# Kernel optimization log

Measured on AMD Instinct MI355X. Metric: run time of the kernel, lower is better.

## Reference

```python
import jax, jax.numpy as jnp
import numpy as np

B, S, E = 4, 4096, 1024
H, D, L = 16, 64, 64   # heads, head_dim, landmarks
KS = 33                # depthwise conv kernel size (seq dim)
N_ITER = 6


def setup_inputs() -> dict:
    key = jax.random.key(0)
    ks = jax.random.split(key, 8)
    s = 0.02
    return {
        "hidden_states": jax.random.normal(ks[0], (B, S, E), dtype=jnp.float32),
        "Wq": jax.random.normal(ks[1], (E, E), dtype=jnp.float32) * s,
        "bq": jnp.zeros((E,), dtype=jnp.float32),
        "Wk": jax.random.normal(ks[2], (E, E), dtype=jnp.float32) * s,
        "bk": jnp.zeros((E,), dtype=jnp.float32),
        "Wv": jax.random.normal(ks[3], (E, E), dtype=jnp.float32) * s,
        "bv": jnp.zeros((E,), dtype=jnp.float32),
        "conv_w": jax.random.normal(ks[4], (H, 1, KS, 1), dtype=jnp.float32) * 0.1,
    }


def _iterative_pinv_original(a, n_iter=N_ITER):
    # a: [B,H,L,L]. Faithful to _pinv_original_nystrom: GLOBAL max over all batches/heads.
    eye = jnp.eye(a.shape[-1], dtype=a.dtype)
    val = a.swapaxes(-1, -2) / jnp.max(jnp.sum(a, axis=-2))
    for _ in range(n_iter):
        kv = a @ val
        val = 0.25 * val @ (13.0 * eye - kv @ (15.0 * eye - kv @ (7.0 * eye - kv)))
    return val


def reference(hidden_states, Wq, bq, Wk, bk, Wv, bv, conv_w):
    scale = D ** -0.25  # divide q and k each by head_dim**0.25

    def heads(x):  # [B,S,E] -> [B,H,S,D]
        return x.reshape(B, S, H, D).transpose(0, 2, 1, 3)

    q = heads(hidden_states @ Wq + bq) * scale
    k = heads(hidden_states @ Wk + bk) * scale
    v = heads(hidden_states @ Wv + bv)

    # landmark means over segments of length S//L
    ql = q.reshape(B, H, L, S // L, D).mean(axis=-2)  # [B,H,L,D]
    kl = k.reshape(B, H, L, S // L, D).mean(axis=-2)  # [B,H,L,D]

    kernel_1 = jax.nn.softmax(jnp.einsum('bhsd,bhld->bhsl', q, kl), axis=-1)   # [B,H,S,L]
    kernel_2 = jax.nn.softmax(jnp.einsum('bhmd,bhld->bhml', ql, kl), axis=-1)  # [B,H,L,L]
    kernel_3 = jax.nn.softmax(jnp.einsum('bhld,bhsd->bhls', ql, k), axis=-1)   # [B,H,L,S]

    pinv = _iterative_pinv_original(kernel_2)
    attention_probs = kernel_1 @ pinv            # [B,H,S,L]
    new_value = kernel_3 @ v                     # [B,H,L,D]
    ctx = attention_probs @ new_value            # [B,H,S,D]

    # depthwise conv skip on value_layer: Conv2d(H,H,(KS,1),groups=H,bias=False)
    pad = KS // 2
    conv_out = jax.lax.conv_general_dilated(
        v, conv_w, window_strides=(1, 1), padding=((pad, pad), (0, 0)),
        dimension_numbers=('NCHW', 'OIHW', 'NCHW'), feature_group_count=H)
    ctx = ctx + conv_out

    return ctx.transpose(0, 2, 1, 3).reshape(B, S, H * D)
```

## Files before the change

kernel.cpp:

```cpp
#include <hip/hip_runtime.h>
#include <stdint.h>

typedef unsigned short u16;
typedef float f32x4 __attribute__((ext_vector_type(4)));
typedef __bf16 bf16x8 __attribute__((ext_vector_type(8)));
typedef u16 u16x8 __attribute__((ext_vector_type(8)));
typedef u16 u16x4 __attribute__((ext_vector_type(4)));

#define SCALE_QK 0.35355339059327373f

#define BAR() asm volatile("s_barrier" ::: "memory")
#define WAIT_LGKM0() do { asm volatile("s_waitcnt lgkmcnt(0)" ::: "memory"); __builtin_amdgcn_sched_barrier(0); } while (0)
#define WAIT_VM(n) do { asm volatile("s_waitcnt vmcnt(" #n ")" ::: "memory"); __builtin_amdgcn_sched_barrier(0); } while (0)

__device__ __forceinline__ u16 f2bf(float f) {
  union { float f; uint32_t u; } x; x.f = f;
  uint32_t r = x.u + 0x7fffu + ((x.u >> 16) & 1u);
  return (u16)(r >> 16);
}
__device__ __forceinline__ float bf2f(u16 h) {
  union { uint32_t u; float f; } x; x.u = ((uint32_t)h) << 16;
  return x.f;
}
__device__ __forceinline__ void gload16(const void* g, void* l) {
  __builtin_amdgcn_global_load_lds((const __attribute__((address_space(1))) void*)g,
                                   (__attribute__((address_space(3))) void*)l, 16, 0, 0);
}
__device__ __forceinline__ bf16x8 ld_f32_to_bf8(const float* p) {
  f32x4 a = *(const f32x4*)p, b = *(const f32x4*)(p + 4);
  union { u16x8 u; bf16x8 h; } c;
  c.u[0] = f2bf(a[0]); c.u[1] = f2bf(a[1]); c.u[2] = f2bf(a[2]); c.u[3] = f2bf(a[3]);
  c.u[4] = f2bf(b[0]); c.u[5] = f2bf(b[1]); c.u[6] = f2bf(b[2]); c.u[7] = f2bf(b[3]);
  return c.h;
}

__global__ __launch_bounds__(256) void k_prep(const float* __restrict__ hidden,
                                              const float* __restrict__ Wq, const float* __restrict__ Wk,
                                              const float* __restrict__ Wv,
                                              u16* __restrict__ hb, u16* __restrict__ Wt) {
  __shared__ float tile[64][65];
  const int bx = blockIdx.x;
  const int t = threadIdx.x;
  if (bx < 8192) {
    const size_t i = ((size_t)bx * 256 + t) * 8;
    f32x4 v0 = *(const f32x4*)(hidden + i);
    f32x4 v1 = *(const f32x4*)(hidden + i + 4);
    u16x8 o;
    o[0] = f2bf(v0[0]); o[1] = f2bf(v0[1]); o[2] = f2bf(v0[2]); o[3] = f2bf(v0[3]);
    o[4] = f2bf(v1[0]); o[5] = f2bf(v1[1]); o[6] = f2bf(v1[2]); o[7] = f2bf(v1[3]);
    *(u16x8*)(hb + i) = o;
    return;
  }
  const int bxx = bx - 8192;
  const int w = bxx >> 8, tn = (bxx >> 4) & 15, tk = bxx & 15;
  const float* W = (w == 0) ? Wq : ((w == 1) ? Wk : Wv);
  const int r = t >> 2, c0 = (t & 3) * 16;
  const float* src = W + (size_t)(tk * 64 + r) * 1024 + tn * 64 + c0;
#pragma unroll
  for (int j = 0; j < 16; j += 4) {
    f32x4 x = *(const f32x4*)(src + j);
    tile[r][c0 + j + 0] = x[0]; tile[r][c0 + j + 1] = x[1];
    tile[r][c0 + j + 2] = x[2]; tile[r][c0 + j + 3] = x[3];
  }
  __syncthreads();
  u16* dst = Wt + (size_t)(w * 1024 + tn * 64 + r) * 1024 + tk * 64 + c0;
#pragma unroll
  for (int j = 0; j < 16; ++j) dst[j] = f2bf(tile[c0 + j][r]);
}

__device__ __forceinline__ bf16x8 frg(const u16* buf, int row, int ks, int lhi) {
  const int ck = (ks << 2) + lhi;
  return *reinterpret_cast<const bf16x8*>(buf + (row << 6) + ((ck ^ (row & 7)) << 3));
}
__device__ __forceinline__ void issue(const u16* g, int rowbase, int tc, u16* ldsbase, int wid) {
  gload16(g + (((size_t)rowbase) << 10) + tc, ldsbase + ((rowbase + (wid << 3)) << 6));
}
template <int Q>
__device__ __forceinline__ void quad_mfma(const bf16x8 (&af)[2][2], const bf16x8 (&bf)[4][2],
                                          f32x4 (&acc)[8][4]) {
#pragma unroll
  for (int mm = 0; mm < 2; ++mm)
#pragma unroll
    for (int n = 0; n < 4; ++n) {
      acc[Q * 2 + mm][n] = __builtin_amdgcn_mfma_f32_16x16x32_bf16(af[mm][0], bf[n][0], acc[Q * 2 + mm][n], 0, 0, 0);
      acc[Q * 2 + mm][n] = __builtin_amdgcn_mfma_f32_16x16x32_bf16(af[mm][1], bf[n][1], acc[Q * 2 + mm][n], 0, 0, 0);
    }
}
#define LOADA_TO(dst, Q)                                     \
  dst[0][0] = frg(ASr, rA0 + (Q)*32, 0, lhi);                \
  dst[0][1] = frg(ASr, rA0 + (Q)*32, 1, lhi);                \
  dst[1][0] = frg(ASr, rA0 + (Q)*32 + 16, 0, lhi);           \
  dst[1][1] = frg(ASr, rA0 + (Q)*32 + 16, 1, lhi);

__global__ __launch_bounds__(512) void k_gemm2(const u16* __restrict__ A, const u16* __restrict__ Bt,
                                               const float* __restrict__ bq, const float* __restrict__ bk,
                                               const float* __restrict__ bv,
                                               u16* __restrict__ oq, u16* __restrict__ ok, u16* __restrict__ ov,
                                               float* __restrict__ ql, float* __restrict__ kl) {
  __shared__ __align__(16) u16 AS[2][256 * 64];
  __shared__ __align__(16) u16 BS[2][256 * 64];
  __shared__ __align__(16) u16 obuf[8][16][70];
  const int t = threadIdx.x, lane = t & 63, wid = t >> 6;
  const int wm = wid >> 2, wn = wid & 3;
  const int bm = blockIdx.x, bn = blockIdx.y;
  const int l15 = lane & 15, lhi = lane >> 4;

  const int rowoff = t >> 3;
  const int cswz = (t & 7) ^ (rowoff & 7);
  const u16* aG = A + (((size_t)(bm * 256 + rowoff)) << 10) + (cswz << 3);
  const u16* bG = Bt + (((size_t)(bn * 256 + rowoff)) << 10) + (cswz << 3);

  const int rA0 = wm * 128 + l15;
  const int rB0 = wn * 64 + l15;

  f32x4 acc[8][4];
#pragma unroll
  for (int m = 0; m < 8; ++m)
#pragma unroll
    for (int n = 0; n < 4; ++n) acc[m][n] = (f32x4){0.f, 0.f, 0.f, 0.f};

  issue(bG, 0, 0, BS[0], wid);
  issue(bG, 64, 0, BS[0], wid);
  issue(bG, 128, 0, BS[0], wid);
  issue(bG, 192, 0, BS[0], wid);
  issue(aG, 0, 0, AS[0], wid);
  issue(aG, 128, 0, AS[0], wid);
  issue(aG, 64, 0, AS[0], wid);
  issue(aG, 192, 0, AS[0], wid);
  WAIT_VM(2);
  BAR();

  for (int u = 0; u < 15; ++u) {
    const int pu = u & 1;
    const u16* ASr = AS[pu];
    const u16* BSr = BS[pu];
    u16* ASw = AS[pu ^ 1];
    u16* BSw = BS[pu ^ 1];
    const int tc = (u + 1) << 6;
    bf16x8 bfr[4][2];
    bf16x8 afA[2][2], afB[2][2];
#pragma unroll
    for (int n = 0; n < 4; ++n) {
      bfr[n][0] = frg(BSr, rB0 + n * 16, 0, lhi);
      bfr[n][1] = frg(BSr, rB0 + n * 16, 1, lhi);
    }
    LOADA_TO(afA, 0)
    LOADA_TO(afB, 1)
    issue(bG, 0, tc, BSw, wid);
    issue(bG, 64, tc, BSw, wid);
    issue(bG, 128, tc, BSw, wid);
    issue(bG, 192, tc, BSw, wid);
    issue(aG, 0, tc, ASw, wid);
    issue(aG, 128, tc, ASw, wid);
    issue(aG, 64, tc, ASw, wid);
    issue(aG, 192, tc, ASw, wid);
    __builtin_amdgcn_s_setprio(1);
    quad_mfma<0>(afA, bfr, acc);
    __builtin_amdgcn_s_setprio(0);
    WAIT_VM(8);
    BAR();
    LOADA_TO(afA, 2)
    __builtin_amdgcn_s_setprio(1);
    quad_mfma<1>(afB, bfr, acc);
    __builtin_amdgcn_s_setprio(0);
    LOADA_TO(afB, 3)
    __builtin_amdgcn_s_setprio(1);
    quad_mfma<2>(afA, bfr, acc);
    __builtin_amdgcn_s_setprio(0);
    __builtin_amdgcn_s_setprio(1);
    quad_mfma<3>(afB, bfr, acc);
    __builtin_amdgcn_s_setprio(0);
    WAIT_VM(2);
    BAR();
  }
  {
    const u16* ASr = AS[1];
    const u16* BSr = BS[1];
    bf16x8 bfr[4][2];
    bf16x8 afA[2][2], afB[2][2];
#pragma unroll
    for (int n = 0; n < 4; ++n) {
      bfr[n][0] = frg(BSr, rB0 + n * 16, 0, lhi);
      bfr[n][1] = frg(BSr, rB0 + n * 16, 1, lhi);
    }
    LOADA_TO(afA, 0)
    LOADA_TO(afB, 1)
    quad_mfma<0>(afA, bfr, acc);
    WAIT_VM(0);
    BAR();
    LOADA_TO(afA, 2)
    quad_mfma<1>(afB, bfr, acc);
    LOADA_TO(afB, 3)
    quad_mfma<2>(afA, bfr, acc);
    quad_mfma<3>(afB, bfr, acc);
  }

  const int which = bn >> 2;
  const float* bias = (which == 0) ? bq : ((which == 1) ? bk : bv);
  u16* op = (which == 0) ? oq : ((which == 1) ? ok : ov);
  const float scl = (which < 2) ? SCALE_QK : 1.0f;
  const int h = ((bn & 3) << 2) + wn;
  const int rowBase2 = (bm << 8) + (wm << 7);
  const int rl = lhi << 2;
  const int srow = lane >> 2, d0 = (lane & 3) * 16;
  float bb[4];
#pragma unroll
  for (int n = 0; n < 4; ++n) bb[n] = bias[((bn & 3) << 8) + (wn << 6) + n * 16 + l15];
#pragma unroll
  for (int m = 0; m < 8; ++m) {
#pragma unroll
    for (int n = 0; n < 4; ++n)
#pragma unroll
      for (int r = 0; r < 4; ++r)
        obuf[wid][rl + r][n * 16 + l15] = f2bf((acc[m][n][r] + bb[n]) * scl);
    const int gm = rowBase2 + m * 16 + srow;
    const int b_ = gm >> 12, s = gm & 4095;
    u16* dst = op + (((size_t)b_ * 16 + h) * 4096 + s) * 64 + d0;
    *(u16x8*)dst = *(const u16x8*)&obuf[wid][srow][d0];
    *(u16x8*)(dst + 8) = *(const u16x8*)&obuf[wid][srow][d0 + 8];
  }
  if (which < 2) {
    float* lmp = (which == 0) ? ql : kl;
    const int bh = ((bm >> 4) << 4) + h;
#pragma unroll
    for (int sg = 0; sg < 2; ++sg) {
#pragma unroll
      for (int n = 0; n < 4; ++n) {
        float s = 0.f;
#pragma unroll
        for (int mi = 0; mi < 4; ++mi)
#pragma unroll
          for (int r = 0; r < 4; ++r) s += (acc[sg * 4 + mi][n][r] + bb[n]) * scl;
        s += __shfl_xor(s, 16, 64);
        s += __shfl_xor(s, 32, 64);
        if (lhi == 0) {
          const int lseg = ((bm & 15) << 2) + (wm << 1) + sg;
          lmp[(size_t)bh * 4096 + lseg * 64 + n * 16 + l15] = s * 0.015625f;
        }
      }
    }
  }
}

__global__ __launch_bounds__(256) void k_k2(const float* __restrict__ ql, const float* __restrict__ kl,
                                            float* __restrict__ k2t, float* __restrict__ colmax,
                                            u16* __restrict__ klb) {
  __shared__ __align__(16) float qlT[64 * 68];
  __shared__ __align__(16) float klT[64 * 68];
  __shared__ __align__(16) float sc[64 * 68];
  const int bh = blockIdx.x, t = threadIdx.x;
  {
    const int r = t >> 2, c0 = (t & 3) * 16;
    const float* qp = ql + (size_t)bh * 4096 + r * 64 + c0;
    const float* kp = kl + (size_t)bh * 4096 + r * 64 + c0;
    u16* kb_ = klb + (size_t)bh * 4096 + r * 64 + c0;
#pragma unroll
    for (int j = 0; j < 16; ++j) {
      qlT[(c0 + j) * 68 + r] = qp[j];
      const float kv = kp[j];
      klT[(c0 + j) * 68 + r] = kv;
      kb_[j] = f2bf(kv);
    }
  }
  __syncthreads();
  {
    const int mg = (t >> 4) * 4, lg = (t & 15) * 4;
    float acc[4][4];
#pragma unroll
    for (int i = 0; i < 4; ++i)
#pragma unroll
      for (int j = 0; j < 4; ++j) acc[i][j] = 0.f;
    for (int d0 = 0; d0 < 64; ++d0) {
      f32x4 x = *(const f32x4*)&qlT[d0 * 68 + mg];
      f32x4 y = *(const f32x4*)&klT[d0 * 68 + lg];
#pragma unroll
      for (int i = 0; i < 4; ++i)
#pragma unroll
        for (int j = 0; j < 4; ++j) acc[i][j] += x[i] * y[j];
    }
#pragma unroll
    for (int i = 0; i < 4; ++i)
#pragma unroll
      for (int j = 0; j < 4; ++j) sc[(mg + i) * 68 + lg + j] = acc[i][j];
  }
  __syncthreads();
  if (t < 64) {
    float mx = -1e30f;
    for (int l = 0; l < 64; ++l) mx = fmaxf(mx, sc[t * 68 + l]);
    float sum = 0.f;
    for (int l = 0; l < 64; ++l) { float e = __expf(sc[t * 68 + l] - mx); sc[t * 68 + l] = e; sum += e; }
    const float inv = 1.0f / sum;
    for (int l = 0; l < 64; ++l) sc[t * 68 + l] *= inv;
  }
  __syncthreads();
  {
    const int r = t >> 2, c0 = (t & 3) * 16;
    float* ot = k2t + (size_t)bh * 4096 + r * 64 + c0;
#pragma unroll
    for (int j = 0; j < 16; ++j) ot[j] = sc[(c0 + j) * 68 + r];
  }
  if (t < 64) {
    float s = 0.f;
    for (int m = 0; m < 64; ++m) s += sc[m * 68 + t];
    for (int off = 32; off; off >>= 1) s = fmaxf(s, __shfl_down(s, off, 64));
    if (t == 0) colmax[bh] = s;
  }
}

__global__ __launch_bounds__(512) void k_pinv(const float* __restrict__ k2t, const float* __restrict__ colmax,
                                              float* __restrict__ pinv) {
  __shared__ float valN[4096];
  __shared__ float kvT[4096];
  __shared__ float t1N[4096];
  __shared__ float t2N[4096];
  __shared__ float gsh;
  const int bh = blockIdx.x, t = threadIdx.x;
  const float* aT = k2t + (size_t)bh * 4096;
  if (t < 64) {
    float v = colmax[t];
    for (int off = 32; off; off >>= 1) v = fmaxf(v, __shfl_down(v, off, 64));
    if (t == 0) gsh = v;
  }
  __syncthreads();
  const float ginv = 1.0f / gsh;
  const int rt = t >> 3, ct0 = (t & 7) * 8;
  {
    const float* p = aT + rt * 64 + ct0;
#pragma unroll
    for (int j = 0; j < 8; ++j) valN[rt * 64 + ct0 + j] = p[j] * ginv;
  }
  __syncthreads();
  const int rg = (t >> 4) * 2, cg = (t & 15) * 4;
  float acc[2][4];
  for (int it = 0; it < 6; ++it) {
#pragma unroll
    for (int i = 0; i < 2; ++i)
#pragma unroll
      for (int j = 0; j < 4; ++j) acc[i][j] = 0.f;
    for (int k = 0; k < 64; ++k) {
      const float x0 = aT[k * 64 + rg], x1 = aT[k * 64 + rg + 1];
      f32x4 y = *(const f32x4*)&valN[k * 64 + cg];
#pragma unroll
      for (int j = 0; j < 4; ++j) { acc[0][j] += x0 * y[j]; acc[1][j] += x1 * y[j]; }
    }
#pragma unroll
    for (int i = 0; i < 2; ++i)
#pragma unroll
      for (int j = 0; j < 4; ++j) kvT[(cg + j) * 64 + rg + i] = acc[i][j];
    __syncthreads();
#pragma unroll
    for (int j = 0; j < 8; ++j) {
      const int c = ct0 + j;
      t1N[rt * 64 + c] = ((rt == c) ? 7.0f : 0.0f) - kvT[c * 64 + rt];
    }
    __syncthreads();
#pragma unroll
    for (int i = 0; i < 2; ++i)
#pragma unroll
      for (int j = 0; j < 4; ++j) acc[i][j] = 0.f;
    for (int k = 0; k < 64; ++k) {
      const float x0 = kvT[k * 64 + rg], x1 = kvT[k * 64 + rg + 1];
      f32x4 y = *(const f32x4*)&t1N[k * 64 + cg];
#pragma unroll
      for (int j = 0; j < 4; ++j) { acc[0][j] += x0 * y[j]; acc[1][j] += x1 * y[j]; }
    }
#pragma unroll
    for (int i = 0; i < 2; ++i)
#pragma unroll
      for (int j = 0; j < 4; ++j) {
        const int r_ = rg + i, c_ = cg + j;
        t2N[r_ * 64 + c_] = ((r_ == c_) ? 15.0f : 0.0f) - acc[i][j];
      }
    __syncthreads();
#pragma unroll
    for (int i = 0; i < 2; ++i)
#pragma unroll
      for (int j = 0; j < 4; ++j) acc[i][j] = 0.f;
    for (int k = 0; k < 64; ++k) {
      const float x0 = kvT[k * 64 + rg], x1 = kvT[k * 64 + rg + 1];
      f32x4 y = *(const f32x4*)&t2N[k * 64 + cg];
#pragma unroll
      for (int j = 0; j < 4; ++j) { acc[0][j] += x0 * y[j]; acc[1][j] += x1 * y[j]; }
    }
#pragma unroll
    for (int i = 0; i < 2; ++i)
#pragma unroll
      for (int j = 0; j < 4; ++j) {
        const int r_ = rg + i, c_ = cg + j;
        t1N[r_ * 64 + c_] = ((r_ == c_) ? 13.0f : 0.0f) - acc[i][j];
      }
    __syncthreads();
#pragma unroll
    for (int j = 0; j < 8; ++j) t2N[(ct0 + j) * 64 + rt] = valN[rt * 64 + ct0 + j];
    __syncthreads();
#pragma unroll
    for (int i = 0; i < 2; ++i)
#pragma unroll
      for (int j = 0; j < 4; ++j) acc[i][j] = 0.f;
    for (int k = 0; k < 64; ++k) {
      const float x0 = t2N[k * 64 + rg], x1 = t2N[k * 64 + rg + 1];
      f32x4 y = *(const f32x4*)&t1N[k * 64 + cg];
#pragma unroll
      for (int j = 0; j < 4; ++j) { acc[0][j] += x0 * y[j]; acc[1][j] += x1 * y[j]; }
    }
#pragma unroll
    for (int i = 0; i < 2; ++i)
#pragma unroll
      for (int j = 0; j < 4; ++j) valN[(rg + i) * 64 + cg + j] = 0.25f * acc[i][j];
    __syncthreads();
  }
  {
    float* o = pinv + (size_t)bh * 4096 + rt * 64 + ct0;
#pragma unroll
    for (int j = 0; j < 8; ++j) o[j] = valN[rt * 64 + ct0 + j];
  }
}

__global__ __launch_bounds__(256) void k_s3nv(const float* __restrict__ ql, const u16* __restrict__ kb,
                                              const u16* __restrict__ vb,
                                              float* __restrict__ nvp, float* __restrict__ zp) {
  __shared__ __align__(16) u16 VT[2][64][72];
  __shared__ __align__(16) u16 e_lds[4][16][72];
  const int bh = blockIdx.x, scn = blockIdx.y;
  const int t = threadIdx.x, lane = t & 63, w = t >> 6;
  const int l15 = lane & 15, kg = (lane >> 4) << 3, rl = (lane >> 4) << 2;
  const float* aRow = ql + (size_t)bh * 4096 + (w * 16 + l15) * 64 + kg;
  bf16x8 aql[2];
  aql[0] = ld_f32_to_bf8(aRow);
  aql[1] = ld_f32_to_bf8(aRow + 32);
  f32x4 accv[4];
#pragma unroll
  for (int n = 0; n < 4; ++n) accv[n] = (f32x4){0.f, 0.f, 0.f, 0.f};
  float zacc[4] = {0.f, 0.f, 0.f, 0.f};
  const int sBase = scn * 512;
  {
    const u16* vp = vb + ((size_t)bh * 4096 + sBase + lane) * 64 + w * 16;
    u16x8 h0 = *(const u16x8*)vp, h1 = *(const u16x8*)(vp + 8);
#pragma unroll
    for (int j = 0; j < 8; ++j) { VT[0][w * 16 + j][lane] = h0[j]; VT[0][w * 16 + 8 + j][lane] = h1[j]; }
  }
  __syncthreads();
  for (int sub = 0; sub < 8; ++sub) {
    const int s0 = sBase + sub * 64;
    u16x8 hn0 = {0,0,0,0,0,0,0,0}, hn1 = {0,0,0,0,0,0,0,0};
    if (sub < 7) {
      const u16* vpn = vb + ((size_t)bh * 4096 + s0 + 64 + lane) * 64 + w * 16;
      hn0 = *(const u16x8*)vpn; hn1 = *(const u16x8*)(vpn + 8);
    }
    const u16* bRow = kb + ((size_t)bh * 4096 + s0 + l15) * 64 + kg;
    f32x4 e[4];
#pragma unroll
    for (int n = 0; n < 4; ++n) e[n] = (f32x4){0.f, 0.f, 0.f, 0.f};
#pragma unroll
    for (int ks = 0; ks < 2; ++ks)
#pragma unroll
      for (int n = 0; n < 4; ++n) {
        bf16x8 bk = *reinterpret_cast<const bf16x8*>(bRow + n * 1024 + ks * 32);
        e[n] = __builtin_amdgcn_mfma_f32_16x16x32_bf16(aql[ks], bk, e[n], 0, 0, 0);
      }
#pragma unroll
    for (int n = 0; n < 4; ++n)
#pragma unroll
      for (int r = 0; r < 4; ++r) {
        const float v = __expf(e[n][r]);
        zacc[r] += v;
        e_lds[w][rl + r][n * 16 + l15] = f2bf(v);
      }
    if (sub < 7) {
      const int nb = (sub + 1) & 1;
#pragma unroll
      for (int j = 0; j < 8; ++j) { VT[nb][w * 16 + j][lane] = hn0[j]; VT[nb][w * 16 + 8 + j][lane] = hn1[j]; }
    }
    WAIT_LGKM0();
    const int cb = sub & 1;
#pragma unroll
    for (int ks = 0; ks < 2; ++ks) {
      bf16x8 af = *reinterpret_cast<const bf16x8*>(&e_lds[w][l15][kg + ks * 32]);
#pragma unroll
      for (int n = 0; n < 4; ++n) {
        bf16x8 bf_ = *reinterpret_cast<const bf16x8*>(&VT[cb][n * 16 + l15][kg + ks * 32]);
        accv[n] = __builtin_amdgcn_mfma_f32_16x16x32_bf16(af, bf_, accv[n], 0, 0, 0);
      }
    }
    BAR();
  }
#pragma unroll
  for (int r = 0; r < 4; ++r)
#pragma unroll
    for (int n = 0; n < 4; ++n)
      nvp[(((size_t)scn * 64 + bh) * 64 + w * 16 + rl + r) * 64 + n * 16 + l15] = accv[n][r];
#pragma unroll
  for (int r = 0; r < 4; ++r) {
    float s = zacc[r];
    s += __shfl_xor(s, 1, 64); s += __shfl_xor(s, 2, 64);
    s += __shfl_xor(s, 4, 64); s += __shfl_xor(s, 8, 64);
    if (l15 == 0) zp[((size_t)scn * 64 + bh) * 64 + w * 16 + rl + r] = s;
  }
}

__global__ __launch_bounds__(256) void k_pnv(const float* __restrict__ pinv, const float* __restrict__ nvp,
                                             const float* __restrict__ zp, u16* __restrict__ Mtb) {
  __shared__ __align__(16) float XT[64 * 68];
  __shared__ __align__(16) float Y[64 * 68];
  const int bh = blockIdx.x, t = threadIdx.x;
  {
    const int r = t >> 2, c0 = (t & 3) * 16;
    const float* pp = pinv + (size_t)bh * 4096 + r * 64 + c0;
#pragma unroll
    for (int j = 0; j < 16; ++j) XT[(c0 + j) * 68 + r] = pp[j];
    float zs = 0.f;
#pragma unroll
    for (int p = 0; p < 8; ++p) zs += zp[((size_t)p * 64 + bh) * 64 + r];
    const float iz = 1.0f / zs;
#pragma unroll
    for (int j = 0; j < 16; ++j) {
      float s = 0.f;
#pragma unroll
      for (int p = 0; p < 8; ++p) s += nvp[(((size_t)p * 64 + bh) * 64 + r) * 64 + c0 + j];
      Y[r * 68 + c0 + j] = s * iz;
    }
  }
  __syncthreads();
  const int rg = (t >> 4) * 4, cg = (t & 15) * 4;
  float acc[4][4];
#pragma unroll
  for (int i = 0; i < 4; ++i)
#pragma unroll
    for (int j = 0; j < 4; ++j) acc[i][j] = 0.f;
  for (int k = 0; k < 64; ++k) {
    f32x4 x = *(const f32x4*)&XT[k * 68 + rg];
    f32x4 y = *(const f32x4*)&Y[k * 68 + cg];
#pragma unroll
    for (int i = 0; i < 4; ++i)
#pragma unroll
      for (int j = 0; j < 4; ++j) acc[i][j] += x[i] * y[j];
  }
#pragma unroll
  for (int j = 0; j < 4; ++j) {
    u16x4 o = {f2bf(acc[0][j]), f2bf(acc[1][j]), f2bf(acc[2][j]), f2bf(acc[3][j])};
    *(u16x4*)&Mtb[(size_t)bh * 4096 + (cg + j) * 64 + rg] = o;
  }
}

__global__ __launch_bounds__(256) void k_out(const u16* __restrict__ qb, const u16* __restrict__ vb,
                                             const u16* __restrict__ klb, const u16* __restrict__ Mtb,
                                             const float* __restrict__ cw, float* __restrict__ out) {
  __shared__ __align__(16) u16 P_lds[4][16][72];
  __shared__ __align__(16) u16 vtile_t[64][100];
  __shared__ float wsh[33];
  const int bid = blockIdx.x;
  const int bh = bid >> 6, st = bid & 63;
  const int b = bh >> 4, h = bh & 15;
  const int t = threadIdx.x, lane = t & 63, w = t >> 6;
  const int sbase = st * 64;
  const int l15 = lane & 15, kg = (lane >> 4) << 3, rl = (lane >> 4) << 2;

  if (t < 33) wsh[t] = cw[h * 33 + t];
  for (int idx = t; idx < 96 * 8; idx += 256) {
    const int row = idx >> 3, c8 = idx & 7;
    const int sg = sbase + row - 16;
    u16x8 val = {0, 0, 0, 0, 0, 0, 0, 0};
    if (sg >= 0 && sg < 4096) val = *(const u16x8*)(vb + ((size_t)bh * 4096 + sg) * 64 + c8 * 8);
#pragma unroll
    for (int j = 0; j < 8; ++j) vtile_t[c8 * 8 + j][row] = val[j];
  }

  f32x4 c1[4];
#pragma unroll
  for (int n = 0; n < 4; ++n) c1[n] = (f32x4){0.f, 0.f, 0.f, 0.f};
  {
    const u16* aRow = qb + ((size_t)bh * 4096 + sbase + w * 16 + l15) * 64 + kg;
    const u16* kRow = klb + (size_t)bh * 4096 + l15 * 64 + kg;
#pragma unroll
    for (int ks = 0; ks < 2; ++ks) {
      bf16x8 af = *reinterpret_cast<const bf16x8*>(aRow + ks * 32);
#pragma unroll
      for (int n = 0; n < 4; ++n) {
        bf16x8 bf_ = *reinterpret_cast<const bf16x8*>(kRow + n * 1024 + ks * 32);
        c1[n] = __builtin_amdgcn_mfma_f32_16x16x32_bf16(af, bf_, c1[n], 0, 0, 0);
      }
    }
  }
  float invZ[4];
  {
    float z[4] = {0.f, 0.f, 0.f, 0.f};
#pragma unroll
    for (int n = 0; n < 4; ++n)
#pragma unroll
      for (int r = 0; r < 4; ++r) { float v = __expf(c1[n][r]); c1[n][r] = v; z[r] += v; }
#pragma unroll
    for (int r = 0; r < 4; ++r) {
      float s = z[r];
      s += __shfl_xor(s, 1, 64); s += __shfl_xor(s, 2, 64);
      s += __shfl_xor(s, 4, 64); s += __shfl_xor(s, 8, 64);
      invZ[r] = 1.0f / s;
    }
#pragma unroll
    for (int n = 0; n < 4; ++n)
#pragma unroll
      for (int r = 0; r < 4; ++r)
        P_lds[w][rl + r][n * 16 + l15] = f2bf(c1[n][r]);
  }
  __syncthreads();
  f32x4 c2[4];
#pragma unroll
  for (int n = 0; n < 4; ++n) c2[n] = (f32x4){0.f, 0.f, 0.f, 0.f};
  {
    const u16* mRow = Mtb + (size_t)bh * 4096 + l15 * 64 + kg;
#pragma unroll
    for (int ks = 0; ks < 2; ++ks) {
      bf16x8 af = *reinterpret_cast<const bf16x8*>(&P_lds[w][l15][kg + ks * 32]);
#pragma unroll
      for (int n = 0; n < 4; ++n) {
        bf16x8 bf_ = *reinterpret_cast<const bf16x8*>(mRow + n * 1024 + ks * 32);
        c2[n] = __builtin_amdgcn_mfma_f32_16x16x32_bf16(af, bf_, c2[n], 0, 0, 0);
      }
    }
  }
  const int base = w * 16 + rl;
#pragma unroll
  for (int n = 0; n < 4; ++n) {
    const int d = n * 16 + l15;
    float vcol[36];
#pragma unroll
    for (int k8 = 0; k8 < 9; ++k8) {
      u16x4 vq = *(const u16x4*)&vtile_t[d][base + k8 * 4];
      vcol[k8 * 4 + 0] = bf2f(vq[0]); vcol[k8 * 4 + 1] = bf2f(vq[1]);
      vcol[k8 * 4 + 2] = bf2f(vq[2]); vcol[k8 * 4 + 3] = bf2f(vq[3]);
    }
    float cv[4] = {0.f, 0.f, 0.f, 0.f};
#pragma unroll
    for (int jt = 0; jt < 33; ++jt) {
      const float ww = wsh[jt];
#pragma unroll
      for (int r = 0; r < 4; ++r) cv[r] += ww * vcol[r + jt];
    }
#pragma unroll
    for (int r = 0; r < 4; ++r) {
      const int sgl = sbase + base + r;
      out[((size_t)b * 4096 + sgl) * 1024 + h * 64 + d] = c2[n][r] * invZ[r] + cv[r];
    }
  }
}

extern "C" void kernel_launch(void* const* d_in, const int* in_sizes, int n_in,
                              void* d_out, int out_size, void* d_ws, size_t ws_size,
                              hipStream_t stream) {
  const float* hidden = (const float*)d_in[0];
  const float* Wq = (const float*)d_in[1];
  const float* bq = (const float*)d_in[2];
  const float* Wk = (const float*)d_in[3];
  const float* bk = (const float*)d_in[4];
  const float* Wv = (const float*)d_in[5];
  const float* bv = (const float*)d_in[6];
  const float* cw = (const float*)d_in[7];
  float* out = (float*)d_out;

  char* ws = (char*)d_ws;
  u16* qb = (u16*)(ws);
  u16* kb = (u16*)(ws + 33554432ull);
  u16* vb = (u16*)(ws + 67108864ull);
  float* ql = (float*)(ws + 100663296ull);
  float* kl = (float*)(ws + 101711872ull);
  float* k2t = (float*)(ws + 102760448ull);
  float* pinvb = (float*)(ws + 103809024ull);
  u16* Mtb = (u16*)(ws + 104857600ull);
  u16* klb = (u16*)(ws + 105381888ull);
  float* stats = (float*)(ws + 106430464ull);
  u16* wt = (u16*)(ws + 106434560ull);
  u16* hb = (u16*)(ws + 112726016ull);
  float* nvp = (float*)(ws + 112726016ull);
  float* zp = (float*)(ws + 121114624ull);

  k_prep<<<8960, 256, 0, stream>>>(hidden, Wq, Wk, Wv, hb, wt);
  k_gemm2<<<dim3(64, 12), 512, 0, stream>>>(hb, wt, bq, bk, bv, qb, kb, vb, ql, kl);
  k_k2<<<64, 256, 0, stream>>>(ql, kl, k2t, stats, klb);
  k_pinv<<<64, 512, 0, stream>>>(k2t, stats, pinvb);
  k_s3nv<<<dim3(64, 8), 256, 0, stream>>>(ql, kb, vb, nvp, zp);
  k_pnv<<<64, 256, 0, stream>>>(pinvb, nvp, zp, Mtb);
  k_out<<<4096, 256, 0, stream>>>(qb, vb, klb, Mtb, cw, out);
  (void)in_sizes; (void)n_in; (void)out_size; (void)ws_size;
}
```

Baseline: 298.1 us.

## Merge pinv and kernel3·V into one launch, swizzle GEMM block order

The iterative pseudo-inverse and the kernel_3·V partial-sum kernels are merged into one launch. The first 64 blocks compute pinv with an XOR-swizzled LDS layout and 8 outputs per thread, and the remaining blocks do the softmax·V partials split into 16 sequence chunks. The point is to let the latency-bound pinv blocks run alongside the streaming work instead of serially, and to remove one kernel launch. The QKV GEMM grid is remapped to 1D with a grouped block order, which may improve L2 reuse. The risks are LDS pressure and more partials for k_pnv to reduce.

```diff
diff --git a/kernel.cpp b/kernel.cpp
--- a/kernel.cpp
+++ b/kernel.cpp
@@ -102,7 +102,9 @@
   __shared__ __align__(16) u16 obuf[8][16][70];
   const int t = threadIdx.x, lane = t & 63, wid = t >> 6;
   const int wm = wid >> 2, wn = wid & 3;
-  const int bm = blockIdx.x, bn = blockIdx.y;
+  const int bi = blockIdx.x;
+  const int bm = ((bi & 7) << 3) + (bi >> 3) / 12;
+  const int bn = (bi >> 3) % 12;
   const int l15 = lane & 15, lhi = lane >> 4;
 
   const int rowoff = t >> 3;
@@ -307,124 +309,114 @@
   }
 }
 
-__global__ __launch_bounds__(512) void k_pinv(const float* __restrict__ k2t, const float* __restrict__ colmax,
-                                              float* __restrict__ pinv) {
-  __shared__ float valN[4096];
-  __shared__ float kvT[4096];
-  __shared__ float t1N[4096];
-  __shared__ float t2N[4096];
+__device__ __forceinline__ int pidx(int row, int c) {
+  return (row << 6) + ((((c >> 2) ^ (row & 15)) << 2) | (c & 3));
+}
+__device__ __forceinline__ void mm64s(const float* __restrict__ X, const float* __restrict__ Y,
+                                      int row, int c0, float* __restrict__ acc) {
+#pragma unroll
+  for (int j = 0; j < 8; ++j) acc[j] = 0.f;
+  for (int kc = 0; kc < 16; ++kc) {
+    f32x4 xq = *(const f32x4*)&X[pidx(row, kc << 2)];
+#pragma unroll
+    for (int kk = 0; kk < 4; ++kk) {
+      const int k = (kc << 2) + kk;
+      f32x4 y0 = *(const f32x4*)&Y[pidx(k, c0)];
+      f32x4 y1 = *(const f32x4*)&Y[pidx(k, c0 + 4)];
+      const float x = xq[kk];
+#pragma unroll
+      for (int j = 0; j < 4; ++j) { acc[j] += x * y0[j]; acc[4 + j] += x * y1[j]; }
+    }
+  }
+}
+
+__global__ __launch_bounds__(512) void k_mid(const float* __restrict__ k2t, const float* __restrict__ colmax,
+                                             float* __restrict__ pinv,
+                                             const float* __restrict__ ql, const u16* __restrict__ kb,
+                                             const u16* __restrict__ vb,
+                                             float* __restrict__ nvp, float* __restrict__ zp) {
+  __shared__ __align__(16) char smem_s[81920];
   __shared__ float gsh;
-  const int bh = blockIdx.x, t = threadIdx.x;
-  const float* aT = k2t + (size_t)bh * 4096;
-  if (t < 64) {
-    float v = colmax[t];
-    for (int off = 32; off; off >>= 1) v = fmaxf(v, __shfl_down(v, off, 64));
-    if (t == 0) gsh = v;
-  }
-  __syncthreads();
-  const float ginv = 1.0f / gsh;
-  const int rt = t >> 3, ct0 = (t & 7) * 8;
-  {
-    const float* p = aT + rt * 64 + ct0;
-#pragma unroll
-    for (int j = 0; j < 8; ++j) valN[rt * 64 + ct0 + j] = p[j] * ginv;
-  }
-  __syncthreads();
-  const int rg = (t >> 4) * 2, cg = (t & 15) * 4;
-  float acc[2][4];
-  for (int it = 0; it < 6; ++it) {
-#pragma unroll
-    for (int i = 0; i < 2; ++i)
-#pragma unroll
-      for (int j = 0; j < 4; ++j) acc[i][j] = 0.f;
-    for (int k = 0; k < 64; ++k) {
-      const float x0 = aT[k * 64 + rg], x1 = aT[k * 64 + rg + 1];
-      f32x4 y = *(const f32x4*)&valN[k * 64 + cg];
-#pragma unroll
-      for (int j = 0; j < 4; ++j) { acc[0][j] += x0 * y[j]; acc[1][j] += x1 * y[j]; }
-    }
-#pragma unroll
-    for (int i = 0; i < 2; ++i)
-#pragma unroll
-      for (int j = 0; j < 4; ++j) kvT[(cg + j) * 64 + rg + i] = acc[i][j];
+  const int t = threadIdx.x;
+  if (blockIdx.x < 64) {
+    float* aS = (float*)smem_s;
+    float* vl = aS + 4096;
+    float* kv = vl + 4096;
+    float* t1 = kv + 4096;
+    float* t2 = t1 + 4096;
+    const int bh = blockIdx.x;
+    const float* aT = k2t + (size_t)bh * 4096;
+    if (t < 64) {
+      float v = colmax[t];
+      for (int off = 32; off; off >>= 1) v = fmaxf(v, __shfl_down(v, off, 64));
+      if (t == 0) gsh = v;
+    }
+    const int row = t >> 3, c0 = (t & 7) << 3;
+#pragma unroll
+    for (int j = 0; j < 8; ++j) {
+      const int i = t * 8 + j;
+      aS[pidx(i & 63, i >> 6)] = aT[i];
+    }
     __syncthreads();
-#pragma unroll
-    for (int j = 0; j < 8; ++j) {
-      const int c = ct0 + j;
-      t1N[rt * 64 + c] = ((rt == c) ? 7.0f : 0.0f) - kvT[c * 64 + rt];
+    const float ginv = 1.0f / gsh;
+    {
+      f32x4 v0 = *(const f32x4*)(aT + row * 64 + c0);
+      f32x4 v1 = *(const f32x4*)(aT + row * 64 + c0 + 4);
+      v0 *= ginv; v1 *= ginv;
+      *(f32x4*)&vl[pidx(row, c0)] = v0;
+      *(f32x4*)&vl[pidx(row, c0 + 4)] = v1;
     }
     __syncthreads();
-#pragma unroll
-    for (int i = 0; i < 2; ++i)
-#pragma unroll
-      for (int j = 0; j < 4; ++j) acc[i][j] = 0.f;
-    for (int k = 0; k < 64; ++k) {
-      const float x0 = kvT[k * 64 + rg], x1 = kvT[k * 64 + rg + 1];
-      f32x4 y = *(const f32x4*)&t1N[k * 64 + cg];
-#pragma unroll
-      for (int j = 0; j < 4; ++j) { acc[0][j] += x0 * y[j]; acc[1][j] += x1 * y[j]; }
-    }
-#pragma unroll
-    for (int i = 0; i < 2; ++i)
-#pragma unroll
-      for (int j = 0; j < 4; ++j) {
-        const int r_ = rg + i, c_ = cg + j;
-        t2N[r_ * 64 + c_] = ((r_ == c_) ? 15.0f : 0.0f) - acc[i][j];
-      }
-    __syncthreads();
-#pragma unroll
-    for (int i = 0; i < 2; ++i)
-#pragma unroll
-      for (int j = 0; j < 4; ++j) acc[i][j] = 0.f;
-    for (int k = 0; k < 64; ++k) {
-      const float x0 = kvT[k * 64 + rg], x1 = kvT[k * 64 + rg + 1];
-      f32x4 y = *(const f32x4*)&t2N[k * 64 + cg];
-#pragma unroll
-      for (int j = 0; j < 4; ++j) { acc[0][j] += x0 * y[j]; acc[1][j] += x1 * y[j]; }
-    }
-#pragma unroll
-    for (int i = 0; i < 2; ++i)
-#pragma unroll
-      for (int j = 0; j < 4; ++j) {
-        const int r_ = rg + i, c_ = cg + j;
-        t1N[r_ * 64 + c_] = ((r_ == c_) ? 13.0f : 0.0f) - acc[i][j];
-      }
-    __syncthreads();
-#pragma unroll
-    for (int j = 0; j < 8; ++j) t2N[(ct0 + j) * 64 + rt] = valN[rt * 64 + ct0 + j];
-    __syncthreads();
-#pragma unroll
-    for (int i = 0; i < 2; ++i)
-#pragma unroll
-      for (int j = 0; j < 4; ++j) acc[i][j] = 0.f;
-    for (int k = 0; k < 64; ++k) {
-      const float x0 = t2N[k * 64 + rg], x1 = t2N[k * 64 + rg + 1];
-      f32x4 y = *(const f32x4*)&t1N[k * 64 + cg];
-#pragma unroll
-      for (int j = 0; j < 4; ++j) { acc[0][j] += x0 * y[j]; acc[1][j] += x1 * y[j]; }
-    }
-#pragma unroll
-    for (int i = 0; i < 2; ++i)
-#pragma unroll
-      for (int j = 0; j < 4; ++j) valN[(rg + i) * 64 + cg + j] = 0.25f * acc[i][j];
-    __syncthreads();
-  }
-  {
-    float* o = pinv + (size_t)bh * 4096 + rt * 64 + ct0;
-#pragma unroll
-    for (int j = 0; j < 8; ++j) o[j] = valN[rt * 64 + ct0 + j];
-  }
-}
-
-__global__ __launch_bounds__(256) void k_s3nv(const float* __restrict__ ql, const u16* __restrict__ kb,
-                                              const u16* __restrict__ vb,
-                                              float* __restrict__ nvp, float* __restrict__ zp) {
-  __shared__ __align__(16) u16 VT[2][64][72];
-  __shared__ __align__(16) u16 e_lds[4][16][72];
-  const int bh = blockIdx.x, scn = blockIdx.y;
-  const int t = threadIdx.x, lane = t & 63, w = t >> 6;
+    float acc[8];
+    for (int it = 0; it < 6; ++it) {
+      mm64s(aS, vl, row, c0, acc);
+#pragma unroll
+      for (int j = 0; j < 8; ++j) kv[pidx(row, c0 + j)] = acc[j];
+      __syncthreads();
+#pragma unroll
+      for (int j = 0; j < 8; ++j) {
+        const int c = c0 + j;
+        t1[pidx(row, c)] = ((row == c) ? 7.0f : 0.0f) - kv[pidx(row, c)];
+      }
+      __syncthreads();
+      mm64s(kv, t1, row, c0, acc);
+#pragma unroll
+      for (int j = 0; j < 8; ++j) {
+        const int c = c0 + j;
+        t2[pidx(row, c)] = ((row == c) ? 15.0f : 0.0f) - acc[j];
+      }
+      __syncthreads();
+      mm64s(kv, t2, row, c0, acc);
+#pragma unroll
+      for (int j = 0; j < 8; ++j) {
+        const int c = c0 + j;
+        t1[pidx(row, c)] = ((row == c) ? 13.0f : 0.0f) - acc[j];
+      }
+      __syncthreads();
+      mm64s(vl, t1, row, c0, acc);
+#pragma unroll
+      for (int j = 0; j < 8; ++j) t2[pidx(row, c0 + j)] = 0.25f * acc[j];
+      __syncthreads();
+#pragma unroll
+      for (int j = 0; j < 8; ++j) vl[pidx(row, c0 + j)] = t2[pidx(row, c0 + j)];
+      __syncthreads();
+    }
+    {
+      f32x4 o0 = *(const f32x4*)&vl[pidx(row, c0)];
+      f32x4 o1 = *(const f32x4*)&vl[pidx(row, c0 + 4)];
+      *(f32x4*)(pinv + (size_t)bh * 4096 + row * 64 + c0) = o0;
+      *(f32x4*)(pinv + (size_t)bh * 4096 + row * 64 + c0 + 4) = o1;
+    }
+    return;
+  }
+  u16* VTs = (u16*)smem_s;
+  u16* els = (u16*)(smem_s + 36864);
+  const int id = (int)blockIdx.x - 64;
+  const int bh = id & 63, scn = id >> 6;
+  const int lane = t & 63, w = t >> 6;
+  const int wq = w & 3, half = w >> 2;
   const int l15 = lane & 15, kg = (lane >> 4) << 3, rl = (lane >> 4) << 2;
-  const float* aRow = ql + (size_t)bh * 4096 + (w * 16 + l15) * 64 + kg;
+  const float* aRow = ql + (size_t)bh * 4096 + (wq * 16 + l15) * 64 + kg;
   bf16x8 aql[2];
   aql[0] = ld_f32_to_bf8(aRow);
   aql[1] = ld_f32_to_bf8(aRow + 32);
@@ -432,19 +424,25 @@
 #pragma unroll
   for (int n = 0; n < 4; ++n) accv[n] = (f32x4){0.f, 0.f, 0.f, 0.f};
   float zacc[4] = {0.f, 0.f, 0.f, 0.f};
-  const int sBase = scn * 512;
-  {
-    const u16* vp = vb + ((size_t)bh * 4096 + sBase + lane) * 64 + w * 16;
+  const int sBase = scn * 512 + half * 256;
+  u16* VT0 = VTs + ((size_t)(0 * 2 + half) * 64) * 72;
+  u16* VT1 = VTs + ((size_t)(1 * 2 + half) * 64) * 72;
+  u16* elw = els + ((size_t)w * 16) * 72;
+  {
+    const u16* vp = vb + ((size_t)bh * 4096 + sBase + lane) * 64 + wq * 16;
     u16x8 h0 = *(const u16x8*)vp, h1 = *(const u16x8*)(vp + 8);
 #pragma unroll
-    for (int j = 0; j < 8; ++j) { VT[0][w * 16 + j][lane] = h0[j]; VT[0][w * 16 + 8 + j][lane] = h1[j]; }
+    for (int j = 0; j < 8; ++j) {
+      VT0[(wq * 16 + j) * 72 + lane] = h0[j];
+      VT0[(wq * 16 + 8 + j) * 72 + lane] = h1[j];
+    }
   }
   __syncthreads();
-  for (int sub = 0; sub < 8; ++sub) {
+  for (int sub = 0; sub < 4; ++sub) {
     const int s0 = sBase + sub * 64;
-    u16x8 hn0 = {0,0,0,0,0,0,0,0}, hn1 = {0,0,0,0,0,0,0,0};
-    if (sub < 7) {
-      const u16* vpn = vb + ((size_t)bh * 4096 + s0 + 64 + lane) * 64 + w * 16;
+    u16x8 hn0 = {0, 0, 0, 0, 0, 0, 0, 0}, hn1 = {0, 0, 0, 0, 0, 0, 0, 0};
+    if (sub < 3) {
+      const u16* vpn = vb + ((size_t)bh * 4096 + s0 + 64 + lane) * 64 + wq * 16;
       hn0 = *(const u16x8*)vpn; hn1 = *(const u16x8*)(vpn + 8);
     }
     const u16* bRow = kb + ((size_t)bh * 4096 + s0 + l15) * 64 + kg;
@@ -455,8 +453,8 @@
     for (int ks = 0; ks < 2; ++ks)
 #pragma unroll
       for (int n = 0; n < 4; ++n) {
-        bf16x8 bk = *reinterpret_cast<const bf16x8*>(bRow + n * 1024 + ks * 32);
-        e[n] = __builtin_amdgcn_mfma_f32_16x16x32_bf16(aql[ks], bk, e[n], 0, 0, 0);
+        bf16x8 bk_ = *reinterpret_cast<const bf16x8*>(bRow + n * 1024 + ks * 32);
+        e[n] = __builtin_amdgcn_mfma_f32_16x16x32_bf16(aql[ks], bk_, e[n], 0, 0, 0);
       }
 #pragma unroll
     for (int n = 0; n < 4; ++n)
@@ -464,37 +462,41 @@
       for (int r = 0; r < 4; ++r) {
         const float v = __expf(e[n][r]);
         zacc[r] += v;
-        e_lds[w][rl + r][n * 16 + l15] = f2bf(v);
-      }
-    if (sub < 7) {
-      const int nb = (sub + 1) & 1;
-#pragma unroll
-      for (int j = 0; j < 8; ++j) { VT[nb][w * 16 + j][lane] = hn0[j]; VT[nb][w * 16 + 8 + j][lane] = hn1[j]; }
+        elw[(rl + r) * 72 + n * 16 + l15] = f2bf(v);
+      }
+    if (sub < 3) {
+      u16* VTn = ((sub + 1) & 1) ? VT1 : VT0;
+#pragma unroll
+      for (int j = 0; j < 8; ++j) {
+        VTn[(wq * 16 + j) * 72 + lane] = hn0[j];
+        VTn[(wq * 16 + 8 + j) * 72 + lane] = hn1[j];
+      }
     }
     WAIT_LGKM0();
-    const int cb = sub & 1;
+    const u16* VTc = (sub & 1) ? VT1 : VT0;
 #pragma unroll
     for (int ks = 0; ks < 2; ++ks) {
-      bf16x8 af = *reinterpret_cast<const bf16x8*>(&e_lds[w][l15][kg + ks * 32]);
+      bf16x8 af = *reinterpret_cast<const bf16x8*>(&elw[l15 * 72 + kg + ks * 32]);
 #pragma unroll
       for (int n = 0; n < 4; ++n) {
-        bf16x8 bf_ = *reinterpret_cast<const bf16x8*>(&VT[cb][n * 16 + l15][kg + ks * 32]);
+        bf16x8 bf_ = *reinterpret_cast<const bf16x8*>(&VTc[(n * 16 + l15) * 72 + kg + ks * 32]);
         accv[n] = __builtin_amdgcn_mfma_f32_16x16x32_bf16(af, bf_, accv[n], 0, 0, 0);
       }
     }
     BAR();
   }
+  const int p = scn * 2 + half;
 #pragma unroll
   for (int r = 0; r < 4; ++r)
 #pragma unroll
     for (int n = 0; n < 4; ++n)
-      nvp[(((size_t)scn * 64 + bh) * 64 + w * 16 + rl + r) * 64 + n * 16 + l15] = accv[n][r];
+      nvp[(((size_t)p * 64 + bh) * 64 + wq * 16 + rl + r) * 64 + n * 16 + l15] = accv[n][r];
 #pragma unroll
   for (int r = 0; r < 4; ++r) {
     float s = zacc[r];
     s += __shfl_xor(s, 1, 64); s += __shfl_xor(s, 2, 64);
     s += __shfl_xor(s, 4, 64); s += __shfl_xor(s, 8, 64);
-    if (l15 == 0) zp[((size_t)scn * 64 + bh) * 64 + w * 16 + rl + r] = s;
+    if (l15 == 0) zp[((size_t)p * 64 + bh) * 64 + wq * 16 + rl + r] = s;
   }
 }
 
@@ -510,13 +512,13 @@
     for (int j = 0; j < 16; ++j) XT[(c0 + j) * 68 + r] = pp[j];
     float zs = 0.f;
 #pragma unroll
-    for (int p = 0; p < 8; ++p) zs += zp[((size_t)p * 64 + bh) * 64 + r];
+    for (int p = 0; p < 16; ++p) zs += zp[((size_t)p * 64 + bh) * 64 + r];
     const float iz = 1.0f / zs;
 #pragma unroll
     for (int j = 0; j < 16; ++j) {
       float s = 0.f;
 #pragma unroll
-      for (int p = 0; p < 8; ++p) s += nvp[(((size_t)p * 64 + bh) * 64 + r) * 64 + c0 + j];
+      for (int p = 0; p < 16; ++p) s += nvp[(((size_t)p * 64 + bh) * 64 + r) * 64 + c0 + j];
       Y[r * 68 + c0 + j] = s * iz;
     }
   }
@@ -670,13 +672,12 @@
   u16* wt = (u16*)(ws + 106434560ull);
   u16* hb = (u16*)(ws + 112726016ull);
   float* nvp = (float*)(ws + 112726016ull);
-  float* zp = (float*)(ws + 121114624ull);
+  float* zp = (float*)(ws + 129503232ull);
 
   k_prep<<<8960, 256, 0, stream>>>(hidden, Wq, Wk, Wv, hb, wt);
-  k_gemm2<<<dim3(64, 12), 512, 0, stream>>>(hb, wt, bq, bk, bv, qb, kb, vb, ql, kl);
+  k_gemm2<<<768, 512, 0, stream>>>(hb, wt, bq, bk, bv, qb, kb, vb, ql, kl);
   k_k2<<<64, 256, 0, stream>>>(ql, kl, k2t, stats, klb);
-  k_pinv<<<64, 512, 0, stream>>>(k2t, stats, pinvb);
-  k_s3nv<<<dim3(64, 8), 256, 0, stream>>>(ql, kb, vb, nvp, zp);
+  k_mid<<<576, 512, 0, stream>>>(k2t, stats, pinvb, ql, kb, vb, nvp, zp);
   k_pnv<<<64, 256, 0, stream>>>(pinvb, nvp, zp, Mtb);
   k_out<<<4096, 256, 0, stream>>>(qb, vb, klb, Mtb, cw, out);
   (void)in_sizes; (void)n_in; (void)out_size; (void)ws_size;
```

New measurement: 318.9 us (median of 5 runs). +7.0%, slower.
